# Performance work log

Measured on AMD Instinct MI355X. Metric: run time of the kernel, lower is better.

## Reference

```python
import jax, jax.numpy as jnp
import numpy as np

# config constants (match init_kwargs)
C = 1024
NH = 16
HS = C // NH
CHUNK = 64          # attn_chunk_size
TOPK = 32           # attn_topk
WINDOW = 4096       # kv_cache_window_size
MIN_KV = 16384      # min_kv_cache_size
MAX_KV = 32768      # max_kv_cache_size
SHORT = 4096        # short_sequence_criteria
CT = 65536          # incoming kv-cache length


def setup_inputs() -> dict:
    key = jax.random.key(0)
    ks = jax.random.split(key, 7)
    s = 1.0 / np.sqrt(C)
    return {
        "x": jax.random.normal(ks[0], (C,), jnp.float32),
        "k_cache": jax.random.normal(ks[1], (1, CT, C), jnp.float32),
        "v_cache": jax.random.normal(ks[2], (1, CT, C), jnp.float32),
        "Wr": jax.random.normal(ks[3], (C, C), jnp.float32) * s,
        "Wk": jax.random.normal(ks[4], (C, C), jnp.float32) * s,
        "Wv": jax.random.normal(ks[5], (C, C), jnp.float32) * s,
        "Wo": jax.random.normal(ks[6], (C, C), jnp.float32) * s,
    }


def _split_heads(t):  # (1, T, C) -> (1, NH, T, HS)
    return t.reshape(1, t.shape[1], NH, HS).transpose(0, 2, 1, 3)


def _update_kv_cache(q, k_cache, v_cache):
    # q: (1,1,C); caches: (1,CT,C). CT > MIN_KV so compression runs.
    past = CT - WINDOW
    kp = _split_heads(k_cache[:, :past])          # (1,NH,past,HS)
    vp = _split_heads(v_cache[:, :past])
    qh = _split_heads(q)                          # (1,NH,1,HS)
    scores = jnp.einsum("bhqd,bhkd->bhqk", qh, kp) / np.sqrt(HS)
    w = jax.nn.softmax(scores, axis=-1)           # (1,NH,1,past)
    vote = w.sum(axis=-2)                         # (1,NH,past)
    keep = MIN_KV - WINDOW                        # per-head tokens kept
    _, idx = jax.lax.top_k(vote, keep)            # (1,NH,keep), descending vote order
    kpc = jnp.take_along_axis(kp, idx[..., None], axis=2)  # (1,NH,keep,HS)
    vpc = jnp.take_along_axis(vp, idx[..., None], axis=2)
    kpc = kpc.transpose(0, 2, 1, 3).reshape(1, keep, C)
    vpc = vpc.transpose(0, 2, 1, 3).reshape(1, keep, C)
    k_new = jnp.concatenate([kpc, k_cache[:, past:]], axis=1)  # (1, MIN_KV, C)
    v_new = jnp.concatenate([vpc, v_cache[:, past:]], axis=1)
    return k_new, v_new


def reference(x, k_cache, v_cache, Wr, Wk, Wv, Wo):
    x2 = x[None, None, :]                         # (1,1,C)
    q = x2 @ Wr.T
    k = x2 @ Wk.T
    v = x2 @ Wv.T

    # CT > MAX_KV -> compress cache (eviction via attention vote per head)
    k_cache, v_cache = _update_kv_cache(q, k_cache, v_cache)
    CT2 = k_cache.shape[1]                        # MIN_KV = 16384 > SHORT -> sparse path

    num_chunks = CT2 // CHUNK
    kc = k_cache.reshape(1, num_chunks, CHUNK, C)
    vc = v_cache.reshape(1, num_chunks, CHUNK, C)
    chunk_key = kc.mean(axis=2)                   # (1,num_chunks,C)
    chunk_score = jnp.einsum("bqc,bkc->bqk", q, chunk_key)
    _, tidx = jax.lax.top_k(chunk_score[0, 0], TOPK)  # (TOPK,)
    topk_k = kc[:, tidx].reshape(1, TOPK * CHUNK, C)
    topk_v = vc[:, tidx].reshape(1, TOPK * CHUNK, C)

    k_comb = jnp.concatenate([topk_k, k], axis=1)  # (1, TOPK*CHUNK+1, C)
    v_comb = jnp.concatenate([topk_v, v], axis=1)

    qh = _split_heads(q)                          # (1,NH,1,HS)
    kh = _split_heads(k_comb)
    vh = _split_heads(v_comb)
    attn = jax.nn.softmax(
        jnp.einsum("bhqd,bhkd->bhqk", qh, kh) / np.sqrt(HS), axis=-1)
    y = jnp.einsum("bhqk,bhkd->bhqd", attn, vh)   # (1,NH,1,HS)
    y = y.transpose(0, 2, 1, 3).reshape(C)
    y = y @ Wo.T
    return y
```

## Files before the change

kernel.cpp:

```cpp
#include <hip/hip_runtime.h>
#include <stdint.h>

#define C      1024
#define NH     16
#define HS     64
#define CT     65536
#define PAST   61440
#define KEEP   12288
#define NCOMP  192
#define NSEL   32
#define NB     8192
#define NBLK   256
#define FLAGW  8

typedef unsigned long long ull;

#define LD_A(p)   __hip_atomic_load((p), __ATOMIC_RELAXED, __HIP_MEMORY_SCOPE_AGENT)
#define ST_A(p,v) __hip_atomic_store((p), (v), __ATOMIC_RELAXED, __HIP_MEMORY_SCOPE_AGENT)

__device__ __forceinline__ unsigned int desc_key(float f) {
    unsigned int b = __float_as_uint(f);
    return (b >> 31) ? b : (~b & 0x7FFFFFFFu);
}
__device__ __forceinline__ float u_to_f(unsigned int u) {
    unsigned int b = (u & 0x80000000u) ? u : (0x7FFFFFFFu - u);
    return __uint_as_float(b);
}
__device__ __forceinline__ int bin_of(float s, float hi, float scale) {
    int b = (int)((hi - s) * scale);
    return b < 0 ? 0 : (b > NB - 1 ? NB - 1 : b);
}
__device__ __forceinline__ void load_params(const unsigned* umin, const unsigned* umax,
                                            int h, float* hi, float* sc) {
    float h2 = u_to_f(umin[h]);
    float lo = u_to_f(umax[h]);
    float r = h2 - lo;
    *hi = h2;
    *sc = (r > 0.f) ? (float)(NB - 1) / r : 0.f;
}

__device__ __forceinline__ void arrive(unsigned* flag, unsigned ph) {
    __syncthreads();
    if (threadIdx.x == 0) {
        asm volatile("s_waitcnt vmcnt(0)" ::: "memory");
        ST_A(&flag[blockIdx.x * FLAGW], ph);
    }
}
__device__ __forceinline__ void wait_head(unsigned* flag, unsigned ph, int h) {
    if (threadIdx.x < 16)
        while (LD_A(&flag[(h * 16 + threadIdx.x) * FLAGW]) < ph)
            __builtin_amdgcn_s_sleep(2);
    __syncthreads();
}
__device__ __forceinline__ void wait_all(unsigned* flag, unsigned ph) {
    if (threadIdx.x < 256)
        while (LD_A(&flag[threadIdx.x * FLAGW]) < ph)
            __builtin_amdgcn_s_sleep(2);
    __syncthreads();
}

__global__ void k_proj(const float* __restrict__ x, const float* __restrict__ Wr,
                       const float* __restrict__ Wk, const float* __restrict__ Wv,
                       float* __restrict__ q, float* __restrict__ kn, float* __restrict__ vn,
                       unsigned* __restrict__ hc, unsigned* __restrict__ umin,
                       unsigned* __restrict__ umax, ull* __restrict__ cs_fix,
                       unsigned* __restrict__ flag) {
    int gid = blockIdx.x * 256 + threadIdx.x;
    for (int i = gid; i < 2 * NH * NB; i += 196608) hc[i] = 0;
    if (blockIdx.x >= 512 && blockIdx.x < 520)
        flag[(blockIdx.x - 512) * 256 + threadIdx.x] = 0u;
    if (blockIdx.x == 700) {
        if (threadIdx.x < 16) umin[threadIdx.x] = 0xFFFFFFFFu;
        else if (threadIdx.x < 32) umax[threadIdx.x - 16] = 0u;
    }
    if (blockIdx.x == 701 && threadIdx.x < 256) cs_fix[threadIdx.x] = 0ull;

    int w = blockIdx.x * (blockDim.x >> 6) + (threadIdx.x >> 6);
    int lane = threadIdx.x & 63;
    int mat = w >> 10, row = w & 1023;
    const float* W = (mat == 0) ? Wr : (mat == 1) ? Wk : Wv;
    const float4* Wrow = (const float4*)(W + (size_t)row * C);
    const float4* x4 = (const float4*)x;
    float acc = 0.f;
#pragma unroll
    for (int i = 0; i < 4; ++i) {
        float4 a = Wrow[i * 64 + lane];
        float4 b = x4[i * 64 + lane];
        acc += a.x * b.x + a.y * b.y + a.z * b.z + a.w * b.w;
    }
#pragma unroll
    for (int off = 32; off; off >>= 1) acc += __shfl_xor(acc, off);
    if (lane == 0) { (mat == 0 ? q : (mat == 1 ? kn : vn))[row] = acc; }
}

__global__ __launch_bounds__(1024, 2) void k_mega(
        const float* __restrict__ kc, const float* __restrict__ vc,
        unsigned* __restrict__ umin, unsigned* __restrict__ umax,
        unsigned* __restrict__ hist, unsigned* __restrict__ cnt,
        ull* __restrict__ G, unsigned* __restrict__ stok,
        ull* __restrict__ cs_fix, float* __restrict__ part,
        const float* __restrict__ q, const float* __restrict__ kn,
        const float* __restrict__ vn, const float* __restrict__ Wo,
        float* __restrict__ yg, float* __restrict__ out,
        float* __restrict__ s, unsigned* __restrict__ flag) {
    const int bid = blockIdx.x, tid = threadIdx.x;
    const int lane = tid & 63, wave = tid >> 6;
    const int h = bid >> 4, seg = bid & 15;
    __shared__ __align__(16) char smem[49664];
    __shared__ unsigned shT, shN;
    __shared__ unsigned wsum[16];
    __shared__ long long wredl[16];

    {
        float (*scl)[16][17] = (float(*)[16][17])smem;
        float* smn = (float*)(smem + 18496);
        float* smx = (float*)(smem + 19520);
        const int t0 = bid * 256 + wave * 16;
        const float4* q4 = (const float4*)q;
        float4 qv[4];
#pragma unroll
        for (int i = 0; i < 4; ++i) qv[i] = q4[i * 64 + lane];
        float mnv[4] = {3.4e38f, 3.4e38f, 3.4e38f, 3.4e38f};
        float mxv[4] = {-3.4e38f, -3.4e38f, -3.4e38f, -3.4e38f};
        for (int tb = 0; tb < 16; tb += 4) {
            float4 av[4][4];
#pragma unroll
            for (int u = 0; u < 4; ++u) {
                const float4* row = (const float4*)(kc + (size_t)(t0 + tb + u) * C);
#pragma unroll
                for (int i = 0; i < 4; ++i) av[u][i] = row[i * 64 + lane];
            }
#pragma unroll
            for (int u = 0; u < 4; ++u) {
                float acc[4];
#pragma unroll
                for (int i = 0; i < 4; ++i)
                    acc[i] = av[u][i].x * qv[i].x + av[u][i].y * qv[i].y
                           + av[u][i].z * qv[i].z + av[u][i].w * qv[i].w;
#pragma unroll
                for (int off = 8; off; off >>= 1) {
#pragma unroll
                    for (int i = 0; i < 4; ++i) acc[i] += __shfl_xor(acc[i], off);
                }
                if ((lane & 15) == 0) {
                    int g = lane >> 4;
#pragma unroll
                    for (int i = 0; i < 4; ++i) {
                        scl[wave][4 * i + g][tb + u] = acc[i];
                        mnv[i] = fminf(mnv[i], acc[i]);
                        mxv[i] = fmaxf(mxv[i], acc[i]);
                    }
                }
            }
        }
        __syncthreads();
        int tt2 = lane & 15;
#pragma unroll
        for (int r = 0; r < 4; ++r) {
            int h2 = r * 4 + (lane >> 4);
            ST_A(&s[(size_t)h2 * CT + t0 + tt2], scl[wave][h2][tt2]);
        }
        if (bid < 240) {
            if ((lane & 15) == 0) {
                int g = lane >> 4;
#pragma unroll
                for (int i = 0; i < 4; ++i) {
                    smn[wave * 16 + 4 * i + g] = mnv[i];
                    smx[wave * 16 + 4 * i + g] = mxv[i];
                }
            }
            __syncthreads();
            if (tid < 16) {
                float mn = smn[tid], mx = smx[tid];
                for (int w2 = 1; w2 < 16; ++w2) {
                    mn = fminf(mn, smn[w2 * 16 + tid]);
                    mx = fmaxf(mx, smx[w2 * 16 + tid]);
                }
                atomicMin(&umin[tid], desc_key(mx));
                atomicMax(&umax[tid], desc_key(mn));
            }
        } else {
            int k = tid >> 8, sub = tid & 255, hh = sub >> 4, tt = sub & 15;
            long long f = 0;
#pragma unroll
            for (int w2 = 0; w2 < 4; ++w2)
                f += llrintf(scl[4 * k + w2][hh][tt] * 16777216.f);
#pragma unroll
            for (int off = 32; off; off >>= 1) f += __shfl_xor(f, off);
            if ((tid & 63) == 0) wredl[wave] = f;
            __syncthreads();
            if ((tid & 255) == 0)
                ST_A(&cs_fix[NCOMP + (bid - 240) * 4 + k],
                     (ull)(wredl[4 * k] + wredl[4 * k + 1] + wredl[4 * k + 2] + wredl[4 * k + 3]));
        }
    }
    arrive(flag, 1); wait_all(flag, 1);

    float hi, sc; load_params(umin, umax, h, &hi, &sc);
    unsigned* lh = (unsigned*)smem;
    float* s_local = (float*)(smem + 32768);

    {
        for (int i = tid; i < NB; i += 1024) lh[i] = 0;
        __syncthreads();
        const float* sh = s + (size_t)h * CT + seg * 3840;
        for (int i = tid; i < 3840; i += 1024) {
            float v = sh[i];
            s_local[i] = v;
            atomicAdd(&lh[bin_of(v, hi, sc)], 1u);
        }
        __syncthreads();
        unsigned* gh = hist + h * NB;
        for (int i = tid; i < NB; i += 1024) {
            unsigned c = lh[i];
            if (c) atomicAdd(&gh[i], c);
        }
    }
    arrive(flag, 2); wait_head(flag, 2, h);

    {
        const unsigned* gh = hist + h * NB;
        unsigned c8[8]; unsigned loc = 0; int b0 = tid * 8;
#pragma unroll
        for (int k = 0; k < 8; ++k) { c8[k] = gh[b0 + k]; loc += c8[k]; }
        unsigned run = loc;
#pragma unroll
        for (int off = 1; off < 64; off <<= 1) {
            unsigned n = __shfl_up(run, off);
            if (lane >= off) run += n;
        }
        if (lane == 63) wsum[wave] = run;
        __syncthreads();
        if (wave == 0 && lane < 16) {
            unsigned v = wsum[lane];
#pragma unroll
            for (int off = 1; off < 16; off <<= 1) {
                unsigned n = __shfl_up(v, off);
                if (lane >= off) v += n;
            }
            wsum[lane] = v;
        }
        __syncthreads();
        unsigned r = run - loc + (wave ? wsum[wave - 1] : 0u);
#pragma unroll
        for (int k = 0; k < 8; ++k) {
            unsigned c = c8[k];
            lh[b0 + k] = r;
            unsigned inc = r + c;
            if (r < KEEP && inc >= KEEP) { shT = (unsigned)(b0 + k); shN = inc; }
            r = inc;
        }
    }
    __syncthreads();
    const unsigned T = shT, ncand = shN;

    {
        unsigned* ch = cnt + h * NB;
        ull* Gh = G + (size_t)h * 65536;
        for (int i = tid; i < 3840; i += 1024) {
            float v = s_local[i];
            int b = bin_of(v, hi, sc);
            if ((unsigned)b <= T) {
                unsigned pos = lh[b] + atomicAdd(&ch[b], 1u);
                ST_A(&Gh[pos], ((ull)desc_key(v) << 16) | (unsigned)(seg * 3840 + i));
            }
        }
    }
    arrive(flag, 3); wait_head(flag, 3, h);

    {
        ull* csl = (ull*)(smem + 48128);
        if (tid < NCOMP) csl[tid] = 0ull;
        __syncthreads();
        const ull* Gh = G + (size_t)h * 65536;
        for (unsigned p = seg * 1024 + tid; p < ncand; p += 16384) {
            ull pk = Gh[p];
            unsigned u = (unsigned)(pk >> 16);
            float v = u_to_f(u);
            int b = bin_of(v, hi, sc);
            unsigned start = lh[b];
            unsigned end = (b == NB - 1) ? ncand : lh[b + 1];
            unsigned rank = start;
            for (unsigned j = start; j < end; ++j) rank += (Gh[j] < pk) ? 1u : 0u;
            if (rank < KEEP) {
                ST_A(&stok[h * KEEP + rank], (unsigned)(pk & 0xFFFFull));
                long long f = llrintf(v * 16777216.f);
                atomicAdd(&csl[rank >> 6], (ull)f);
            }
        }
        __syncthreads();
        if (tid < NCOMP) {
            ull c = csl[tid];
            if (c) atomicAdd(&cs_fix[tid], c);
        }
    }
    arrive(flag, 4); wait_all(flag, 4);

    {
        ull* key = (ull*)smem;
        unsigned* sel_l = (unsigned*)(smem + 2048);
        float* scm = (float*)(smem + 2176);
        float* exb = (float*)(smem + 2688);
        float* vbuf = (float*)(smem + 3200);
        if (tid < 256) {
            long long v = (long long)cs_fix[tid];
            ull bb = (ull)(v + (1ll << 45));
            key[tid] = (((1ull << 46) - bb) << 8) | (unsigned)tid;
        }
        __syncthreads();
        for (unsigned k = 2; k <= 256; k <<= 1) {
            for (unsigned j = k >> 1; j > 0; j >>= 1) {
                if (tid < 256) {
                    unsigned ixj = tid ^ j;
                    if (ixj > (unsigned)tid) {
                        ull a = key[tid], b = key[ixj];
                        bool up = ((tid & k) == 0);
                        if (up ? (a > b) : (a < b)) { key[tid] = b; key[ixj] = a; }
                    }
                }
                __syncthreads();
            }
        }
        if (tid < NSEL) sel_l[tid] = (unsigned)(key[tid] & 0xFFull);
        __syncthreads();

        int su = tid >> 9, sid = tid & 511;
        int p = bid * 2 + su;
        int hh = p >> 5, ci = p & 31;
        int c = (int)sel_l[ci];
        int g = sid >> 3, q8 = sid & 7;
        int t = (c < NCOMP) ? (int)stok[hh * KEEP + c * 64 + g]
                            : (PAST + (c - NCOMP) * 64 + g);
        if (q8 == 0) scm[su * 64 + g] = s[(size_t)hh * CT + t] * 0.125f;
        __syncthreads();
        float m = -1e30f;
        for (int j = 0; j < 64; ++j) m = fmaxf(m, scm[su * 64 + j]);
        float e = expf(scm[su * 64 + g] - m);
        if (q8 == 0) exb[su * 64 + g] = e;
        const float4* vrow = (const float4*)(vc + (size_t)t * C + hh * HS);
        float4 v0 = vrow[q8 * 2], v1 = vrow[q8 * 2 + 1];
        float* vb = vbuf + su * 4352 + g * 68 + q8 * 8;
        vb[0] = e * v0.x; vb[1] = e * v0.y; vb[2] = e * v0.z; vb[3] = e * v0.w;
        vb[4] = e * v1.x; vb[5] = e * v1.y; vb[6] = e * v1.z; vb[7] = e * v1.w;
        __syncthreads();
        if (sid < 64) {
            float acc = 0.f;
            for (int g2 = 0; g2 < 64; ++g2) acc += vbuf[su * 4352 + g2 * 68 + sid];
            float* P = part + (size_t)(hh * 32 + ci) * 68;
            ST_A(&P[2 + sid], acc);
            if (sid == 0) {
                float es = 0.f;
                for (int g2 = 0; g2 < 64; ++g2) es += exb[su * 64 + g2];
                ST_A(&P[0], m);
                ST_A(&P[1], es);
            }
        }
    }
    arrive(flag, 5); wait_head(flag, 5, h);

    int row = bid * 4 + (wave >> 2), qtr = wave & 3;
    const float4* Wrow4 = (const float4*)(Wo + (size_t)row * C) + qtr * 64;
    float4 wa = Wrow4[lane];

    if (seg == 0 && tid < 64) {
        float p = q[h * 64 + tid] * kn[h * 64 + tid];
#pragma unroll
        for (int off = 32; off; off >>= 1) p += __shfl_xor(p, off);
        float a_new = p * 0.125f;
        const float* P0 = part + (size_t)h * 32 * 68;
        float m = a_new;
        for (int ci = 0; ci < 32; ++ci) m = fmaxf(m, P0[ci * 68]);
        float den = expf(a_new - m);
        float acc = den * vn[h * HS + tid];
        for (int ci = 0; ci < 32; ++ci) {
            float w = expf(P0[ci * 68] - m);
            den += w * P0[ci * 68 + 1];
            acc += w * P0[ci * 68 + 2 + tid];
        }
        ST_A(&yg[h * HS + tid], acc / den);
    }
    if (seg == 0) arrive(flag, 6);
    if (tid < 16)
        while (LD_A(&flag[(tid * 16) * FLAGW]) < 6u) __builtin_amdgcn_s_sleep(2);
    __syncthreads();

    {
        float* yl = (float*)smem;
        float* ps = (float*)(smem + 4096);
        yl[tid] = yg[tid];
        __syncthreads();
        const float4* y4 = (const float4*)yl + qtr * 64;
        float4 b = y4[lane];
        float acc = wa.x * b.x + wa.y * b.y + wa.z * b.z + wa.w * b.w;
#pragma unroll
        for (int off = 32; off; off >>= 1) acc += __shfl_xor(acc, off);
        if (lane == 0) ps[wave] = acc;
        __syncthreads();
        if (tid < 4)
            out[bid * 4 + tid] = ps[tid * 4] + ps[tid * 4 + 1] + ps[tid * 4 + 2] + ps[tid * 4 + 3];
    }
}

extern "C" void kernel_launch(void* const* d_in, const int* in_sizes, int n_in,
                              void* d_out, int out_size, void* d_ws, size_t ws_size,
                              hipStream_t stream) {
    const float* x  = (const float*)d_in[0];
    const float* kc = (const float*)d_in[1];
    const float* vc = (const float*)d_in[2];
    const float* Wr = (const float*)d_in[3];
    const float* Wk = (const float*)d_in[4];
    const float* Wv = (const float*)d_in[5];
    const float* Wo = (const float*)d_in[6];
    float* out = (float*)d_out;
    char* ws = (char*)d_ws;

    float* q    = (float*)(ws + 0);
    float* kn   = (float*)(ws + 8192);
    float* vn   = (float*)(ws + 16384);
    ull* cs_fix = (ull*)(ws + 32768);
    float* yg   = (float*)(ws + 40960);
    float* part = (float*)(ws + 49152);
    unsigned* stok = (unsigned*)(ws + 196608);
    unsigned* umin = (unsigned*)(ws + 1048576);
    unsigned* umax = (unsigned*)(ws + 1048640);
    unsigned* flag = (unsigned*)(ws + 1048832);
    unsigned* hist = (unsigned*)(ws + 1114112);
    unsigned* cnt  = (unsigned*)(ws + 1638400);
    float* s = (float*)(ws + 2621440);
    ull* G = (ull*)(ws + 7340032);

    k_proj<<<768, 256, 0, stream>>>(x, Wr, Wk, Wv, q, kn, vn, hist, umin, umax, cs_fix, flag);
    k_mega<<<NBLK, 1024, 0, stream>>>(kc, vc, umin, umax, hist, cnt, G, stok, cs_fix,
                                      part, q, kn, vn, Wo, yg, out, s, flag);
}
```

Before: 117.0 us.

## Repartition score phase per head-segment, keep scores in LDS, drop global score buffer

Each block now computes scores for its own head over a 4096-token segment instead of all heads over 256 tokens. The scores stay in shared memory for the histogram and candidate-scatter phases, so the full global score array and the wait-for-all barrier after phase 1 are replaced by a per-head wait. Only the window scores go to global memory. The selected tokens' packed key+index values are stored so the final phase recovers the score without re-reading it. The risk is that the per-head strided 256-byte K reads are less coalesced than the earlier full-row reads, and the last segment per head now does only window work, so load is uneven.

```diff
diff --git a/kernel.cpp b/kernel.cpp
--- a/kernel.cpp
+++ b/kernel.cpp
@@ -97,123 +97,93 @@
         const float* __restrict__ kc, const float* __restrict__ vc,
         unsigned* __restrict__ umin, unsigned* __restrict__ umax,
         unsigned* __restrict__ hist, unsigned* __restrict__ cnt,
-        ull* __restrict__ G, unsigned* __restrict__ stok,
+        ull* __restrict__ G, ull* __restrict__ stokv,
         ull* __restrict__ cs_fix, float* __restrict__ part,
         const float* __restrict__ q, const float* __restrict__ kn,
         const float* __restrict__ vn, const float* __restrict__ Wo,
         float* __restrict__ yg, float* __restrict__ out,
-        float* __restrict__ s, unsigned* __restrict__ flag) {
+        float* __restrict__ s_win, unsigned* __restrict__ flag) {
     const int bid = blockIdx.x, tid = threadIdx.x;
     const int lane = tid & 63, wave = tid >> 6;
     const int h = bid >> 4, seg = bid & 15;
-    __shared__ __align__(16) char smem[49664];
+    __shared__ __align__(16) char smem[50688];
     __shared__ unsigned shT, shN;
     __shared__ unsigned wsum[16];
-    __shared__ long long wredl[16];
-
-    {
-        float (*scl)[16][17] = (float(*)[16][17])smem;
-        float* smn = (float*)(smem + 18496);
-        float* smx = (float*)(smem + 19520);
-        const int t0 = bid * 256 + wave * 16;
-        const float4* q4 = (const float4*)q;
-        float4 qv[4];
-#pragma unroll
-        for (int i = 0; i < 4; ++i) qv[i] = q4[i * 64 + lane];
-        float mnv[4] = {3.4e38f, 3.4e38f, 3.4e38f, 3.4e38f};
-        float mxv[4] = {-3.4e38f, -3.4e38f, -3.4e38f, -3.4e38f};
-        for (int tb = 0; tb < 16; tb += 4) {
-            float4 av[4][4];
+    __shared__ float smn[16], smx[16];
+
+    float* s_lds = (float*)smem;
+    unsigned* lh = (unsigned*)(smem + 16384);
+
+    {
+        const int t_base = seg * 4096;
+        const int g = lane >> 4;
+        float4 qv = ((const float4*)q)[h * 16 + (lane & 15)];
+        float mn = 3.4e38f, mx = -3.4e38f;
+        for (int ib = 0; ib < 64; ib += 4) {
+            float4 av[4];
 #pragma unroll
             for (int u = 0; u < 4; ++u) {
-                const float4* row = (const float4*)(kc + (size_t)(t0 + tb + u) * C);
-#pragma unroll
-                for (int i = 0; i < 4; ++i) av[u][i] = row[i * 64 + lane];
+                int lt = wave * 256 + (ib + u) * 4 + g;
+                av[u] = ((const float4*)(kc + (size_t)(t_base + lt) * C + h * HS))[lane & 15];
             }
 #pragma unroll
             for (int u = 0; u < 4; ++u) {
-                float acc[4];
-#pragma unroll
-                for (int i = 0; i < 4; ++i)
-                    acc[i] = av[u][i].x * qv[i].x + av[u][i].y * qv[i].y
-                           + av[u][i].z * qv[i].z + av[u][i].w * qv[i].w;
-#pragma unroll
-                for (int off = 8; off; off >>= 1) {
-#pragma unroll
-                    for (int i = 0; i < 4; ++i) acc[i] += __shfl_xor(acc[i], off);
+                float d = av[u].x * qv.x + av[u].y * qv.y + av[u].z * qv.z + av[u].w * qv.w;
+#pragma unroll
+                for (int off = 8; off; off >>= 1) d += __shfl_xor(d, off);
+                int lt = wave * 256 + (ib + u) * 4 + g;
+                if ((lane & 15) == 0) s_lds[lt] = d;
+                mn = fminf(mn, d);
+                mx = fmaxf(mx, d);
+            }
+        }
+        __syncthreads();
+        if (seg < 15) {
+#pragma unroll
+            for (int off = 32; off; off >>= 1) {
+                mn = fminf(mn, __shfl_xor(mn, off));
+                mx = fmaxf(mx, __shfl_xor(mx, off));
+            }
+            if (lane == 0) { smn[wave] = mn; smx[wave] = mx; }
+            __syncthreads();
+            if (tid == 0) {
+                float bmn = smn[0], bmx = smx[0];
+                for (int w2 = 1; w2 < 16; ++w2) {
+                    bmn = fminf(bmn, smn[w2]);
+                    bmx = fmaxf(bmx, smx[w2]);
                 }
-                if ((lane & 15) == 0) {
-                    int g = lane >> 4;
-#pragma unroll
-                    for (int i = 0; i < 4; ++i) {
-                        scl[wave][4 * i + g][tb + u] = acc[i];
-                        mnv[i] = fminf(mnv[i], acc[i]);
-                        mxv[i] = fmaxf(mxv[i], acc[i]);
-                    }
-                }
-            }
-        }
-        __syncthreads();
-        int tt2 = lane & 15;
-#pragma unroll
-        for (int r = 0; r < 4; ++r) {
-            int h2 = r * 4 + (lane >> 4);
-            ST_A(&s[(size_t)h2 * CT + t0 + tt2], scl[wave][h2][tt2]);
-        }
-        if (bid < 240) {
-            if ((lane & 15) == 0) {
-                int g = lane >> 4;
-#pragma unroll
-                for (int i = 0; i < 4; ++i) {
-                    smn[wave * 16 + 4 * i + g] = mnv[i];
-                    smx[wave * 16 + 4 * i + g] = mxv[i];
-                }
-            }
+                atomicMin(&umin[h], desc_key(bmx));
+                atomicMax(&umax[h], desc_key(bmn));
+            }
+        } else {
+            for (int i = tid; i < 4096; i += 1024)
+                ST_A(&s_win[h * 4096 + i], s_lds[i]);
+            int c = tid >> 4;
+            long long f = 0;
+#pragma unroll
+            for (int j = 0; j < 4; ++j)
+                f += llrintf(s_lds[c * 64 + (tid & 15) * 4 + j] * 16777216.f);
+#pragma unroll
+            for (int off = 8; off; off >>= 1) f += __shfl_xor(f, off);
+            if ((tid & 15) == 0) atomicAdd(&cs_fix[NCOMP + c], (ull)f);
+        }
+    }
+    arrive(flag, 1); wait_head(flag, 1, h);
+
+    float hi, sc; load_params(umin, umax, h, &hi, &sc);
+
+    {
+        for (int i = tid; i < NB; i += 1024) lh[i] = 0;
+        __syncthreads();
+        if (seg < 15) {
+            for (int i = tid; i < 4096; i += 1024)
+                atomicAdd(&lh[bin_of(s_lds[i], hi, sc)], 1u);
             __syncthreads();
-            if (tid < 16) {
-                float mn = smn[tid], mx = smx[tid];
-                for (int w2 = 1; w2 < 16; ++w2) {
-                    mn = fminf(mn, smn[w2 * 16 + tid]);
-                    mx = fmaxf(mx, smx[w2 * 16 + tid]);
-                }
-                atomicMin(&umin[tid], desc_key(mx));
-                atomicMax(&umax[tid], desc_key(mn));
-            }
-        } else {
-            int k = tid >> 8, sub = tid & 255, hh = sub >> 4, tt = sub & 15;
-            long long f = 0;
-#pragma unroll
-            for (int w2 = 0; w2 < 4; ++w2)
-                f += llrintf(scl[4 * k + w2][hh][tt] * 16777216.f);
-#pragma unroll
-            for (int off = 32; off; off >>= 1) f += __shfl_xor(f, off);
-            if ((tid & 63) == 0) wredl[wave] = f;
-            __syncthreads();
-            if ((tid & 255) == 0)
-                ST_A(&cs_fix[NCOMP + (bid - 240) * 4 + k],
-                     (ull)(wredl[4 * k] + wredl[4 * k + 1] + wredl[4 * k + 2] + wredl[4 * k + 3]));
-        }
-    }
-    arrive(flag, 1); wait_all(flag, 1);
-
-    float hi, sc; load_params(umin, umax, h, &hi, &sc);
-    unsigned* lh = (unsigned*)smem;
-    float* s_local = (float*)(smem + 32768);
-
-    {
-        for (int i = tid; i < NB; i += 1024) lh[i] = 0;
-        __syncthreads();
-        const float* sh = s + (size_t)h * CT + seg * 3840;
-        for (int i = tid; i < 3840; i += 1024) {
-            float v = sh[i];
-            s_local[i] = v;
-            atomicAdd(&lh[bin_of(v, hi, sc)], 1u);
-        }
-        __syncthreads();
-        unsigned* gh = hist + h * NB;
-        for (int i = tid; i < NB; i += 1024) {
-            unsigned c = lh[i];
-            if (c) atomicAdd(&gh[i], c);
+            unsigned* gh = hist + h * NB;
+            for (int i = tid; i < NB; i += 1024) {
+                unsigned c = lh[i];
+                if (c) atomicAdd(&gh[i], c);
+            }
         }
     }
     arrive(flag, 2); wait_head(flag, 2, h);
@@ -254,22 +224,23 @@
     __syncthreads();
     const unsigned T = shT, ncand = shN;
 
-    {
+    if (seg < 15) {
         unsigned* ch = cnt + h * NB;
         ull* Gh = G + (size_t)h * 65536;
-        for (int i = tid; i < 3840; i += 1024) {
-            float v = s_local[i];
+        const int t_base = seg * 4096;
+        for (int i = tid; i < 4096; i += 1024) {
+            float v = s_lds[i];
             int b = bin_of(v, hi, sc);
             if ((unsigned)b <= T) {
                 unsigned pos = lh[b] + atomicAdd(&ch[b], 1u);
-                ST_A(&Gh[pos], ((ull)desc_key(v) << 16) | (unsigned)(seg * 3840 + i));
+                ST_A(&Gh[pos], ((ull)desc_key(v) << 16) | (unsigned)(t_base + i));
             }
         }
     }
     arrive(flag, 3); wait_head(flag, 3, h);
 
     {
-        ull* csl = (ull*)(smem + 48128);
+        ull* csl = (ull*)(smem + 49152);
         if (tid < NCOMP) csl[tid] = 0ull;
         __syncthreads();
         const ull* Gh = G + (size_t)h * 65536;
@@ -283,7 +254,7 @@
             unsigned rank = start;
             for (unsigned j = start; j < end; ++j) rank += (Gh[j] < pk) ? 1u : 0u;
             if (rank < KEEP) {
-                ST_A(&stok[h * KEEP + rank], (unsigned)(pk & 0xFFFFull));
+                ST_A(&stokv[h * KEEP + rank], pk);
                 long long f = llrintf(v * 16777216.f);
                 atomicAdd(&csl[rank >> 6], (ull)f);
             }
@@ -329,9 +300,17 @@
         int hh = p >> 5, ci = p & 31;
         int c = (int)sel_l[ci];
         int g = sid >> 3, q8 = sid & 7;
-        int t = (c < NCOMP) ? (int)stok[hh * KEEP + c * 64 + g]
-                            : (PAST + (c - NCOMP) * 64 + g);
-        if (q8 == 0) scm[su * 64 + g] = s[(size_t)hh * CT + t] * 0.125f;
+        int t; float sv;
+        if (c < NCOMP) {
+            ull pk = stokv[hh * KEEP + c * 64 + g];
+            t = (int)(pk & 0xFFFFull);
+            sv = u_to_f((unsigned)(pk >> 16));
+        } else {
+            int j = (c - NCOMP) * 64 + g;
+            t = PAST + j;
+            sv = s_win[hh * 4096 + j];
+        }
+        if (q8 == 0) scm[su * 64 + g] = sv * 0.125f;
         __syncthreads();
         float m = -1e30f;
         for (int j = 0; j < 64; ++j) m = fmaxf(m, scm[su * 64 + j]);
@@ -420,16 +399,16 @@
     ull* cs_fix = (ull*)(ws + 32768);
     float* yg   = (float*)(ws + 40960);
     float* part = (float*)(ws + 49152);
-    unsigned* stok = (unsigned*)(ws + 196608);
-    unsigned* umin = (unsigned*)(ws + 1048576);
-    unsigned* umax = (unsigned*)(ws + 1048640);
-    unsigned* flag = (unsigned*)(ws + 1048832);
-    unsigned* hist = (unsigned*)(ws + 1114112);
-    unsigned* cnt  = (unsigned*)(ws + 1638400);
-    float* s = (float*)(ws + 2621440);
-    ull* G = (ull*)(ws + 7340032);
+    unsigned* umin = (unsigned*)(ws + 188416);
+    unsigned* umax = (unsigned*)(ws + 188480);
+    unsigned* flag = (unsigned*)(ws + 192512);
+    float* s_win   = (float*)(ws + 262144);
+    ull* stokv     = (ull*)(ws + 524288);
+    unsigned* hist = (unsigned*)(ws + 2097152);
+    unsigned* cnt  = (unsigned*)(ws + 2621440);
+    ull* G = (ull*)(ws + 3145728);
 
     k_proj<<<768, 256, 0, stream>>>(x, Wr, Wk, Wv, q, kn, vn, hist, umin, umax, cs_fix, flag);
-    k_mega<<<NBLK, 1024, 0, stream>>>(kc, vc, umin, umax, hist, cnt, G, stok, cs_fix,
-                                      part, q, kn, vn, Wo, yg, out, s, flag);
-}
+    k_mega<<<NBLK, 1024, 0, stream>>>(kc, vc, umin, umax, hist, cnt, G, stokv, cs_fix,
+                                      part, q, kn, vn, Wo, yg, out, s_win, flag);
+}
```

After: 115.5 us. About the same (-1.3%).
